# Performance work log

Hardware: AMD Instinct MI355X
Metric: run time of the kernel (lower is better)

The kernel has to match this reference:

```python
import jax, jax.numpy as jnp
import numpy as np

B, L, D = 4, 2048, 512
CHUNK = 64
EPS = 1e-5


def setup_inputs() -> dict:
    key = jax.random.key(0)
    kx, kw = jax.random.split(key)
    x = jax.random.normal(kx, (B, L, D), dtype=jnp.float32)
    W = jax.random.normal(kw, (D, D), dtype=jnp.float32) / np.float32(np.sqrt(D))
    return {
        "x": x,
        "W": W,
        "eta": jnp.asarray(0.01, jnp.float32),
        "lam_logit": jnp.asarray(np.log(0.99 / 0.01), jnp.float32),  # logit(0.99)
        "ln_gamma": jnp.ones((D,), jnp.float32),
        "ln_beta": jnp.zeros((D,), jnp.float32),
    }


def _gated_delta_scan(k, v, q, lam, beta):
    """Gated delta rule: S_t = lam*S_{t-1} + beta * k_t (x) (v_t - lam*S_{t-1}^T k_t);
    o_t = S_t^T q_t (scale=1.0, single head of dim D). k,v,q: [B,L,D] -> o: [B,L,D]."""
    b, l, d = k.shape
    nc = l // CHUNK

    def to_scan(t):  # [B,L,D] -> [nc, CHUNK, B, D]
        return t.transpose(1, 0, 2).reshape(nc, CHUNK, b, d)

    ks, vs, qs = to_scan(k), to_scan(v), to_scan(q)

    def step(S, inp):
        k_t, v_t, q_t = inp                      # each [B,D]
        S = lam * S                              # scalar decay exp(g), g = log(lam)
        v_err = beta * (v_t - jnp.einsum('bk,bkv->bv', k_t, S))
        S = S + k_t[:, :, None] * v_err[:, None, :]
        o_t = jnp.einsum('bk,bkv->bv', q_t, S)
        return S, o_t

    def chunk_body(S, ch):
        return jax.lax.scan(step, S, ch)

    S0 = jnp.zeros((b, d, d), k.dtype)
    _, o = jax.lax.scan(chunk_body, S0, (ks, vs, qs))  # o: [nc, CHUNK, B, D]
    return o.reshape(l, b, d).transpose(1, 0, 2)


def reference(x, W, eta, lam_logit, ln_gamma, ln_beta):
    lam = jax.nn.sigmoid(lam_logit)
    x_act = jnp.tanh(x)
    static_out = jnp.einsum('bld,ed->ble', x_act, W)  # torch Linear (no bias): x @ W.T
    # k = q = tanh(x), v = W @ tanh(x), g = log(lam), beta = eta
    o_dyn = _gated_delta_scan(x_act, static_out, x_act, lam, eta)
    y = static_out + o_dyn
    mu = jnp.mean(y, axis=-1, keepdims=True)
    var = jnp.var(y, axis=-1, keepdims=True)
    return (y - mu) * jax.lax.rsqrt(var + EPS) * ln_gamma + ln_beta
```

## Files before the change

### kernel.cpp

```cpp
#include <hip/hip_runtime.h>
#include <math.h>

#define BB 4
#define LL 2048
#define DD 512
#define CC 64
#define NC 32
#define VB 8
#define EPSF 1e-5f

typedef unsigned int u32;
typedef unsigned short u16;
typedef __attribute__((ext_vector_type(4))) u32 u32x4;
typedef __attribute__((ext_vector_type(4))) float f32x4;
typedef __attribute__((ext_vector_type(8))) __bf16 bf16x8;

__device__ __forceinline__ u16 f2bf(float f) {
  return __builtin_bit_cast(u16, (__bf16)f);
}
__device__ __forceinline__ int sx6(int s) { return (s ^ (s >> 3)) & 7; }
__device__ __forceinline__ bf16x8 ldf(const u16* p) {
  return __builtin_bit_cast(bf16x8, *(const u32x4*)p);
}
__device__ __forceinline__ bf16x8 bcv(u32x4 v) { return __builtin_bit_cast(bf16x8, v); }

__device__ __forceinline__ void gld16(u16* lds, const u16* g) {
  __builtin_amdgcn_global_load_lds(
      (const __attribute__((address_space(1))) u32*)g,
      (__attribute__((address_space(3))) u32*)lds, 16, 0, 0);
}
__device__ __forceinline__ void barrier_lgkm() {
  asm volatile("s_waitcnt lgkmcnt(0)" ::: "memory");
  __builtin_amdgcn_sched_barrier(0);
  __builtin_amdgcn_s_barrier();
  __builtin_amdgcn_sched_barrier(0);
}
__device__ __forceinline__ void barrier_all() {
  asm volatile("s_waitcnt vmcnt(0) lgkmcnt(0)" ::: "memory");
  __builtin_amdgcn_sched_barrier(0);
  __builtin_amdgcn_s_barrier();
  __builtin_amdgcn_sched_barrier(0);
}

__global__ __launch_bounds__(256) void k_tanh(const float* __restrict__ x,
                                              u16* __restrict__ kbs) {
  int row  = blockIdx.x * 4 + (threadIdx.x >> 6);
  int lane = threadIdx.x & 63;
  const float* xr = x + (size_t)row * DD + lane * 8;
  float4 a = *(const float4*)xr;
  float4 b = *(const float4*)(xr + 4);
  float v[8] = {a.x, a.y, a.z, a.w, b.x, b.y, b.z, b.w};
  u32x4 pk;
#pragma unroll
  for (int j = 0; j < 4; ++j) {
    u16 h0 = f2bf(tanhf(v[2 * j]));
    u16 h1 = f2bf(tanhf(v[2 * j + 1]));
    pk[j] = (u32)h0 | ((u32)h1 << 16);
  }
  int s = row & 63;
  int k0 = (lane * 8) ^ (sx6(s) << 3);
  *(u32x4*)(kbs + (size_t)row * DD + k0) = pk;
}

__global__ __launch_bounds__(256) void k_cvtW(const float* __restrict__ W,
                                              u16* __restrict__ wbb) {
  int idx = (blockIdx.x * 256 + threadIdx.x) * 8;
  float4 a = *(const float4*)(W + idx);
  float4 b = *(const float4*)(W + idx + 4);
  float v[8] = {a.x, a.y, a.z, a.w, b.x, b.y, b.z, b.w};
  u32x4 pk;
#pragma unroll
  for (int j = 0; j < 4; ++j)
    pk[j] = (u32)f2bf(v[2 * j]) | ((u32)f2bf(v[2 * j + 1]) << 16);
  *(u32x4*)(wbb + idx) = pk;
}

__global__ __launch_bounds__(256) void k_prep2(const u16* __restrict__ kbs,
                                               const float* __restrict__ eta_p,
                                               const float* __restrict__ ll_p,
                                               u16* __restrict__ tbb,
                                               u16* __restrict__ tcb,
                                               u16* __restrict__ mtb,
                                               u16* __restrict__ kbt) {
  __shared__ __align__(16) u16 Kl[CC * DD];
  __shared__ float Gl[64 * 64];
  __shared__ float Gs[64 * 64];
  __shared__ float Tl[64 * 65];
  __shared__ float pw[72];
  int bc = blockIdx.x;
  int b = bc >> 5, c = bc & 31;
  int tid = threadIdx.x;
  int wid = tid >> 6, lane = tid & 63;
  int lo = lane & 15, hi = lane >> 4;
  float beta = *eta_p;
  float lam = 1.f / (1.f + expf(-*ll_p));
  if (tid <= 64) pw[tid] = powf(lam, (float)tid);
  for (int i = tid; i < 64 * 65; i += 256) Tl[i] = 0.f;
  const u16* Kg = kbs + (size_t)(b * LL + c * CC) * DD;
#pragma unroll
  for (int i = 0; i < 16; ++i)
    gld16(Kl + (size_t)(i * 256 + tid) * 8, Kg + (size_t)(i * 256 + tid) * 8);
  __syncthreads();
  {
    f32x4 acc[4] = {{0.f,0.f,0.f,0.f},{0.f,0.f,0.f,0.f},{0.f,0.f,0.f,0.f},{0.f,0.f,0.f,0.f}};
    int t = 16 * wid + lo;
    int mT = sx6(t) << 3;
#pragma unroll
    for (int kq = 0; kq < 16; ++kq) {
      int col = hi * 8 + kq * 32;
      bf16x8 aF = ldf(Kl + t * DD + (col ^ mT));
#pragma unroll
      for (int sb = 0; sb < 4; ++sb) {
        int s = 16 * sb + lo;
        bf16x8 bF = ldf(Kl + s * DD + (col ^ (sx6(s) << 3)));
        acc[sb] = __builtin_amdgcn_mfma_f32_16x16x32_bf16(aF, bF, acc[sb], 0, 0, 0);
      }
    }
#pragma unroll
    for (int sb = 0; sb < 4; ++sb)
#pragma unroll
      for (int r = 0; r < 4; ++r)
        Gl[(16 * wid + 4 * hi + r) * 64 + 16 * sb + lo] = acc[sb][r];
  }
  __syncthreads();
#pragma unroll
  for (int i = 0; i < 16; ++i) {
    int idx = tid + i * 256;
    int tq = idx >> 6, sq = idx & 63;
    Gs[idx] = (sq < tq) ? beta * pw[tq - sq] * Gl[idx] : 0.f;
  }
  __syncthreads();
  {
    int q = hi;
    int j = 16 * wid + lo;
    for (int t = 0; t < 64; ++t) {
      float ps = 0.f;
#pragma unroll
      for (int i = 0; i < 16; ++i) {
        int s = 16 * q + i;
        ps = fmaf(Gs[t * 64 + s], Tl[s * 65 + j], ps);
      }
      ps += __shfl_xor(ps, 16, 64);
      ps += __shfl_xor(ps, 32, 64);
      if (q == 0) Tl[t * 65 + j] = ((t == j) ? 1.f : 0.f) - ps;
    }
  }
  __syncthreads();
  u16* tb = tbb + (size_t)bc * 64 * 64;
  u16* tc = tcb + (size_t)bc * 64 * 64;
  u16* mt = mtb + (size_t)bc * 64 * 64;
#pragma unroll
  for (int i = 0; i < 16; ++i) {
    int idx = tid + i * 256;
    int s = idx >> 6, r = idx & 63;
    float tv = Tl[s * 65 + r];
    tb[idx] = f2bf(beta * tv);
    tc[idx] = f2bf(-(beta * tv * pw[r + 1]));
    mt[idx] = f2bf((r < s) ? pw[s - r] * Gl[s * 64 + r]
                           : ((r == s) ? Gl[s * 64 + r] : 0.f));
  }
  u16* ktb = kbt + (size_t)bc * CC * DD;
#pragma unroll
  for (int rr = 0; rr < 2; ++rr) {
    int k = rr * 256 + tid;
    int kbase = k & ~7, klo = k & 7;
    int mk = sx6(k) << 3;
#pragma unroll
    for (int g = 0; g < 8; ++g) {
      u32 w4[4];
#pragma unroll
      for (int p = 0; p < 4; ++p) {
        int s0 = g * 8 + 2 * p;
        u16 e0 = Kl[s0 * DD + (kbase ^ (sx6(s0) << 3)) + klo];
        u16 e1 = Kl[(s0 + 1) * DD + (kbase ^ (sx6(s0 + 1) << 3)) + klo];
        w4[p] = (u32)e0 | ((u32)e1 << 16);
      }
      *(u32x4*)(ktb + (size_t)k * 64 + ((8 * g) ^ mk)) = (u32x4){w4[0], w4[1], w4[2], w4[3]};
    }
  }
}

__global__ __launch_bounds__(512, 2) void k_scan6(const u16* __restrict__ kbs,
                                                  const u16* __restrict__ kbt,
                                                  const u16* __restrict__ wbb,
                                                  const u16* __restrict__ tbb,
                                                  const u16* __restrict__ tcb,
                                                  const u16* __restrict__ mtb,
                                                  const float* __restrict__ ll_p,
                                                  float* __restrict__ y) {
  __shared__ __align__(16) u16 Kl[CC * DD];
  __shared__ __align__(16) u16 Sb[16 * DD];
  __shared__ float Vp[2 * 16 * 68];
  __shared__ float Up[2 * 16 * 68];
  __shared__ __align__(16) u16 Vt[16 * 64];
  __shared__ __align__(16) u16 Ut[16 * 64];
  __shared__ __align__(16) u16 Wt[16 * 64];
  __shared__ __align__(16) u16 Ws[16 * 64];

  int b = blockIdx.x >> 6;
  int vb = blockIdx.x & 63;
  int v0 = vb * VB;
  int tid = threadIdx.x;
  int wid = tid >> 6, lane = tid & 63;
  int wq = wid & 3, kh = wid >> 2;
  int lo = lane & 15, hi = lane >> 4;
  int sidx = 16 * wq + lo;
  int mK = sx6(sidx) << 3;
  int mLo = sx6(lo) << 3;
  int kOff = kh * 256;

  float lam = 1.f / (1.f + expf(-*ll_p));
  float lam64 = powf(lam, 64.f);
  float csc = powf(lam, (float)(sidx + 1));
  float dsc = powf(lam, (float)(63 - sidx));

  {
    u32x4 z = {0u, 0u, 0u, 0u};
    *((u32x4*)Sb + tid) = z;
    *((u32x4*)Sb + 512 + tid) = z;
    if (tid < 512) {
      u16* base = (tid >> 7) == 0 ? Vt : (tid >> 7) == 1 ? Ut : (tid >> 7) == 2 ? Wt : Ws;
      *((u32x4*)base + (tid & 127)) = z;
    }
  }
  const u16* kb_b = kbs + (size_t)b * LL * DD;
  float* yb = y + (size_t)b * LL * DD;

  u32x4 wf[8];
#pragma unroll
  for (int kq = 0; kq < 8; ++kq)
    wf[kq] = *(const u32x4*)(wbb + (size_t)((v0 + lo) & 511) * DD + kOff + hi * 8 + kq * 32);

  u32x4 sreg[8];
#pragma unroll
  for (int i = 0; i < 8; ++i)
    sreg[i] = *(const u32x4*)(kb_b + (size_t)(i * 512 + tid) * 8);
  u32x4 kt0[4], kt1[4], tA0, tA1, tB0, tB1;
  {
    const u16* ktc = kbt + (size_t)(b * NC + 0) * CC * DD;
#pragma unroll
    for (int t = 0; t < 4; ++t) {
      int k = 16 * (8 * wq + 4 * kh + t) + lo;
      const u16* rowp = ktc + (size_t)k * 64;
      int m = sx6(k) << 3;
      kt0[t] = *(const u32x4*)(rowp + ((8 * hi) ^ m));
      kt1[t] = *(const u32x4*)(rowp + ((8 * hi + 32) ^ m));
    }
    size_t tbase = ((size_t)(b * NC + 0) * 64 + sidx) * 64 + hi * 8;
    if (kh == 0) {
      tA0 = *(const u32x4*)(tbb + tbase);
      tA1 = *(const u32x4*)(tbb + tbase + 32);
      tB0 = *(const u32x4*)(tcb + tbase);
      tB1 = *(const u32x4*)(tcb + tbase + 32);
    } else {
      tA0 = *(const u32x4*)(mtb + tbase);
      tA1 = *(const u32x4*)(mtb + tbase + 32);
      tB0 = tA0; tB1 = tA1;
    }
  }
#pragma unroll
  for (int i = 0; i < 8; ++i)
    *(u32x4*)(Kl + (size_t)(i * 512 + tid) * 8) = sreg[i];

  f32x4 Sa[4];
#pragma unroll
  for (int t = 0; t < 4; ++t) Sa[t] = (f32x4){0.f, 0.f, 0.f, 0.f};
  barrier_all();

  for (int c = 0; c < NC; ++c) {
    if (c + 1 < NC) {
      const u16* src = kb_b + (size_t)(c + 1) * CC * DD;
#pragma unroll
      for (int i = 0; i < 8; ++i)
        sreg[i] = *(const u32x4*)(src + (size_t)(i * 512 + tid) * 8);
    }
    f32x4 Va0 = {0.f,0.f,0.f,0.f}, Va1 = {0.f,0.f,0.f,0.f};
    f32x4 Ua0 = {0.f,0.f,0.f,0.f}, Ua1 = {0.f,0.f,0.f,0.f};
#pragma unroll
    for (int kq = 0; kq < 8; ++kq) {
      int col = kOff + hi * 8 + kq * 32;
      bf16x8 kB = ldf(Kl + sidx * DD + (col ^ mK));
      bf16x8 sA = ldf(Sb + lo * DD + (col ^ mLo));
      if (kq & 1) {
        Va1 = __builtin_amdgcn_mfma_f32_16x16x32_bf16(bcv(wf[kq]), kB, Va1, 0, 0, 0);
        Ua1 = __builtin_amdgcn_mfma_f32_16x16x32_bf16(sA, kB, Ua1, 0, 0, 0);
      } else {
        Va0 = __builtin_amdgcn_mfma_f32_16x16x32_bf16(bcv(wf[kq]), kB, Va0, 0, 0, 0);
        Ua0 = __builtin_amdgcn_mfma_f32_16x16x32_bf16(sA, kB, Ua0, 0, 0, 0);
      }
    }
#pragma unroll
    for (int r = 0; r < 4; ++r) {
      int v = 4 * hi + r;
      Vp[(kh * 16 + v) * 68 + sidx] = Va0[r] + Va1[r];
      Up[(kh * 16 + v) * 68 + sidx] = Ua0[r] + Ua1[r];
    }
    barrier_lgkm();
    if (c + 1 < NC) {
#pragma unroll
      for (int i = 0; i < 8; ++i)
        *(u32x4*)(Kl + (size_t)(i * 512 + tid) * 8) = sreg[i];
    }
    float VaF[4], UaF[4];
#pragma unroll
    for (int r = 0; r < 4; ++r) {
      int v = 4 * hi + r;
      VaF[r] = Vp[v * 68 + sidx] + Vp[(16 + v) * 68 + sidx];
      UaF[r] = Up[v * 68 + sidx] + Up[(16 + v) * 68 + sidx];
    }
    if (kh == 0 && hi < 2) {
#pragma unroll
      for (int r = 0; r < 4; ++r) {
        int v = 4 * hi + r;
        int idx = v * 64 + (sidx ^ (sx6(v) << 3));
        Vt[idx] = f2bf(VaF[r]);
        Ut[idx] = f2bf(UaF[r]);
      }
    }
    barrier_lgkm();
    if (kh == 0) {
      bf16x8 vf0 = ldf(Vt + lo * 64 + ((hi * 8) ^ mLo));
      bf16x8 vf1 = ldf(Vt + lo * 64 + ((hi * 8 + 32) ^ mLo));
      bf16x8 uf0 = ldf(Ut + lo * 64 + ((hi * 8) ^ mLo));
      bf16x8 uf1 = ldf(Ut + lo * 64 + ((hi * 8 + 32) ^ mLo));
      f32x4 Wa0 = {0.f,0.f,0.f,0.f}, Wa1 = {0.f,0.f,0.f,0.f};
      Wa0 = __builtin_amdgcn_mfma_f32_16x16x32_bf16(vf0, bcv(tA0), Wa0, 0, 0, 0);
      Wa1 = __builtin_amdgcn_mfma_f32_16x16x32_bf16(vf1, bcv(tA1), Wa1, 0, 0, 0);
      Wa0 = __builtin_amdgcn_mfma_f32_16x16x32_bf16(uf0, bcv(tB0), Wa0, 0, 0, 0);
      Wa1 = __builtin_amdgcn_mfma_f32_16x16x32_bf16(uf1, bcv(tB1), Wa1, 0, 0, 0);
      f32x4 Wa = Wa0 + Wa1;
      if (hi < 2) {
#pragma unroll
        for (int r = 0; r < 4; ++r) {
          int v = 4 * hi + r;
          int idx = v * 64 + (sidx ^ (sx6(v) << 3));
          Wt[idx] = f2bf(Wa[r]);
          Ws[idx] = f2bf(Wa[r] * dsc);
        }
      }
    }
    barrier_lgkm();
    if (kh == 1) {
      f32x4 Oa;
#pragma unroll
      for (int r = 0; r < 4; ++r) Oa[r] = csc * UaF[r];
      bf16x8 wff0 = ldf(Wt + lo * 64 + ((hi * 8) ^ mLo));
      bf16x8 wff1 = ldf(Wt + lo * 64 + ((hi * 8 + 32) ^ mLo));
      Oa = __builtin_amdgcn_mfma_f32_16x16x32_bf16(wff0, bcv(tA0), Oa, 0, 0, 0);
      Oa = __builtin_amdgcn_mfma_f32_16x16x32_bf16(wff1, bcv(tA1), Oa, 0, 0, 0);
      if (hi < 2) {
        float4 yo = make_float4(VaF[0] + Oa[0], VaF[1] + Oa[1],
                                VaF[2] + Oa[2], VaF[3] + Oa[3]);
        *(float4*)(yb + (size_t)(c * CC + sidx) * DD + v0 + 4 * hi) = yo;
      }
    }
    {
      bf16x8 ws0 = ldf(Ws + lo * 64 + ((hi * 8) ^ mLo));
      bf16x8 ws1 = ldf(Ws + lo * 64 + ((hi * 8 + 32) ^ mLo));
#pragma unroll
      for (int t = 0; t < 4; ++t) {
        f32x4 acc = Sa[t] * lam64;
        acc = __builtin_amdgcn_mfma_f32_16x16x32_bf16(ws0, bcv(kt0[t]), acc, 0, 0, 0);
        acc = __builtin_amdgcn_mfma_f32_16x16x32_bf16(ws1, bcv(kt1[t]), acc, 0, 0, 0);
        Sa[t] = acc;
      }
      if (hi < 2) {
#pragma unroll
        for (int t = 0; t < 4; ++t) {
          int kc = 16 * (8 * wq + 4 * kh + t) + lo;
#pragma unroll
          for (int r = 0; r < 4; ++r) {
            int v = 4 * hi + r;
            Sb[v * DD + (kc ^ (sx6(v) << 3))] = f2bf(Sa[t][r]);
          }
        }
      }
    }
    if (c + 1 < NC) {
      const u16* ktc = kbt + (size_t)(b * NC + c + 1) * CC * DD;
#pragma unroll
      for (int t = 0; t < 4; ++t) {
        int k = 16 * (8 * wq + 4 * kh + t) + lo;
        const u16* rowp = ktc + (size_t)k * 64;
        int m = sx6(k) << 3;
        kt0[t] = *(const u32x4*)(rowp + ((8 * hi) ^ m));
        kt1[t] = *(const u32x4*)(rowp + ((8 * hi + 32) ^ m));
      }
      size_t tbase = ((size_t)(b * NC + c + 1) * 64 + sidx) * 64 + hi * 8;
      if (kh == 0) {
        tA0 = *(const u32x4*)(tbb + tbase);
        tA1 = *(const u32x4*)(tbb + tbase + 32);
        tB0 = *(const u32x4*)(tcb + tbase);
        tB1 = *(const u32x4*)(tcb + tbase + 32);
      } else {
        tA0 = *(const u32x4*)(mtb + tbase);
        tA1 = *(const u32x4*)(mtb + tbase + 32);
      }
    }
    barrier_lgkm();
  }
}

__global__ __launch_bounds__(256) void k_ln(float* __restrict__ y,
                                            const float* __restrict__ gamma,
                                            const float* __restrict__ lbeta) {
  int row = blockIdx.x * 4 + (threadIdx.x >> 6);
  int lane = threadIdx.x & 63;
  float* yr = y + (size_t)row * DD + lane * 8;
  float4 a = *(const float4*)yr;
  float4 b = *(const float4*)(yr + 4);
  float v[8] = {a.x, a.y, a.z, a.w, b.x, b.y, b.z, b.w};
  float s = 0.f, ss = 0.f;
#pragma unroll
  for (int j = 0; j < 8; ++j) {
    s += v[j];
    ss = fmaf(v[j], v[j], ss);
  }
#pragma unroll
  for (int m = 1; m < 64; m <<= 1) {
    s += __shfl_xor(s, m, 64);
    ss += __shfl_xor(ss, m, 64);
  }
  float mu = s * (1.f / DD);
  float var = ss * (1.f / DD) - mu * mu;
  float inv = rsqrtf(var + EPSF);
  const float* gp = gamma + lane * 8;
  const float* bp = lbeta + lane * 8;
  float4 g0 = *(const float4*)gp;
  float4 g1 = *(const float4*)(gp + 4);
  float4 b0 = *(const float4*)bp;
  float4 b1 = *(const float4*)(bp + 4);
  float g[8] = {g0.x, g0.y, g0.z, g0.w, g1.x, g1.y, g1.z, g1.w};
  float bb[8] = {b0.x, b0.y, b0.z, b0.w, b1.x, b1.y, b1.z, b1.w};
#pragma unroll
  for (int j = 0; j < 8; ++j) v[j] = (v[j] - mu) * inv * g[j] + bb[j];
  *(float4*)yr = make_float4(v[0], v[1], v[2], v[3]);
  *(float4*)(yr + 4) = make_float4(v[4], v[5], v[6], v[7]);
}

extern "C" void kernel_launch(void* const* d_in, const int* in_sizes, int n_in,
                              void* d_out, int out_size, void* d_ws, size_t ws_size,
                              hipStream_t stream) {
  const float* x     = (const float*)d_in[0];
  const float* W     = (const float*)d_in[1];
  const float* eta   = (const float*)d_in[2];
  const float* ll    = (const float*)d_in[3];
  const float* gamma = (const float*)d_in[4];
  const float* lbeta = (const float*)d_in[5];
  float* out = (float*)d_out;

  u16* kbs = (u16*)d_ws;
  u16* kbt = kbs + (size_t)BB * LL * DD;
  u16* wbb = kbt + (size_t)BB * LL * DD;
  u16* tbb = wbb + (size_t)DD * DD;
  u16* tcb = tbb + (size_t)BB * NC * 64 * 64;
  u16* mtb = tcb + (size_t)BB * NC * 64 * 64;

  k_tanh<<<2048, 256, 0, stream>>>(x, kbs);
  k_cvtW<<<128, 256, 0, stream>>>(W, wbb);
  k_prep2<<<BB * NC, 256, 0, stream>>>(kbs, eta, ll, tbb, tcb, mtb, kbt);
  k_scan6<<<256, 512, 0, stream>>>(kbs, kbt, wbb, tbb, tcb, mtb, ll, out);
  k_ln<<<2048, 256, 0, stream>>>(out, gamma, lbeta);
}
```

Measured before the change: 148.9 us.

## Double scan block to 1024 threads and hoist next-chunk V projection off critical path

The scan kernel now runs 16 waves per block instead of 8, splitting the K dimension four ways (128 columns each) and reducing partial sums across four slices in shared memory. The projection V = W·k for the next chunk is computed early, after the current chunk's U/V reduction, so only the S·k product stays on the serial per-chunk path. This roughly halves per-wave MFMA and register work per chunk. In exchange it adds a wider cross-wave reduction, a larger shared buffer, and more threads at each barrier.

```diff
diff --git a/kernel.cpp b/kernel.cpp
--- a/kernel.cpp
+++ b/kernel.cpp
@@ -180,18 +180,18 @@
   }
 }
 
-__global__ __launch_bounds__(512, 2) void k_scan6(const u16* __restrict__ kbs,
-                                                  const u16* __restrict__ kbt,
-                                                  const u16* __restrict__ wbb,
-                                                  const u16* __restrict__ tbb,
-                                                  const u16* __restrict__ tcb,
-                                                  const u16* __restrict__ mtb,
-                                                  const float* __restrict__ ll_p,
-                                                  float* __restrict__ y) {
+__global__ __launch_bounds__(1024, 4) void k_scan7(const u16* __restrict__ kbs,
+                                                   const u16* __restrict__ kbt,
+                                                   const u16* __restrict__ wbb,
+                                                   const u16* __restrict__ tbb,
+                                                   const u16* __restrict__ tcb,
+                                                   const u16* __restrict__ mtb,
+                                                   const float* __restrict__ ll_p,
+                                                   float* __restrict__ y) {
   __shared__ __align__(16) u16 Kl[CC * DD];
   __shared__ __align__(16) u16 Sb[16 * DD];
-  __shared__ float Vp[2 * 16 * 68];
-  __shared__ float Up[2 * 16 * 68];
+  __shared__ float Vp[4 * 16 * 68];
+  __shared__ float Up[4 * 16 * 68];
   __shared__ __align__(16) u16 Vt[16 * 64];
   __shared__ __align__(16) u16 Ut[16 * 64];
   __shared__ __align__(16) u16 Wt[16 * 64];
@@ -207,7 +207,7 @@
   int sidx = 16 * wq + lo;
   int mK = sx6(sidx) << 3;
   int mLo = sx6(lo) << 3;
-  int kOff = kh * 256;
+  int kOff = kh * 128;
 
   float lam = 1.f / (1.f + expf(-*ll_p));
   float lam64 = powf(lam, 64.f);
@@ -217,30 +217,30 @@
   {
     u32x4 z = {0u, 0u, 0u, 0u};
     *((u32x4*)Sb + tid) = z;
-    *((u32x4*)Sb + 512 + tid) = z;
     if (tid < 512) {
-      u16* base = (tid >> 7) == 0 ? Vt : (tid >> 7) == 1 ? Ut : (tid >> 7) == 2 ? Wt : Ws;
+      u16* base = (tid >> 7) == 0 ? Vt : (tid >> 7) == 1 ? Ut
+                : (tid >> 7) == 2 ? Wt : Ws;
       *((u32x4*)base + (tid & 127)) = z;
     }
   }
   const u16* kb_b = kbs + (size_t)b * LL * DD;
   float* yb = y + (size_t)b * LL * DD;
 
-  u32x4 wf[8];
-#pragma unroll
-  for (int kq = 0; kq < 8; ++kq)
+  u32x4 wf[4];
+#pragma unroll
+  for (int kq = 0; kq < 4; ++kq)
     wf[kq] = *(const u32x4*)(wbb + (size_t)((v0 + lo) & 511) * DD + kOff + hi * 8 + kq * 32);
 
-  u32x4 sreg[8];
-#pragma unroll
-  for (int i = 0; i < 8; ++i)
-    sreg[i] = *(const u32x4*)(kb_b + (size_t)(i * 512 + tid) * 8);
-  u32x4 kt0[4], kt1[4], tA0, tA1, tB0, tB1;
+  u32x4 sreg[4];
+#pragma unroll
+  for (int i = 0; i < 4; ++i)
+    sreg[i] = *(const u32x4*)(kb_b + (size_t)(i * 1024 + tid) * 8);
+  u32x4 kt0[2], kt1[2], tA0, tA1, tB0, tB1;
   {
     const u16* ktc = kbt + (size_t)(b * NC + 0) * CC * DD;
 #pragma unroll
-    for (int t = 0; t < 4; ++t) {
-      int k = 16 * (8 * wq + 4 * kh + t) + lo;
+    for (int t = 0; t < 2; ++t) {
+      int k = 16 * (2 * wid + t) + lo;
       const u16* rowp = ktc + (size_t)k * 64;
       int m = sx6(k) << 3;
       kt0[t] = *(const u32x4*)(rowp + ((8 * hi) ^ m));
@@ -259,62 +259,75 @@
     }
   }
 #pragma unroll
-  for (int i = 0; i < 8; ++i)
-    *(u32x4*)(Kl + (size_t)(i * 512 + tid) * 8) = sreg[i];
-
-  f32x4 Sa[4];
-#pragma unroll
-  for (int t = 0; t < 4; ++t) Sa[t] = (f32x4){0.f, 0.f, 0.f, 0.f};
+  for (int i = 0; i < 4; ++i)
+    *(u32x4*)(Kl + (size_t)(i * 1024 + tid) * 8) = sreg[i];
+
+  f32x4 Sa[2];
+  Sa[0] = (f32x4){0.f, 0.f, 0.f, 0.f};
+  Sa[1] = (f32x4){0.f, 0.f, 0.f, 0.f};
   barrier_all();
+
+  {
+    f32x4 Va0 = {0.f,0.f,0.f,0.f}, Va1 = {0.f,0.f,0.f,0.f};
+#pragma unroll
+    for (int kq = 0; kq < 4; ++kq) {
+      int col = kOff + hi * 8 + kq * 32;
+      bf16x8 kB = ldf(Kl + sidx * DD + (col ^ mK));
+      if (kq & 1) Va1 = __builtin_amdgcn_mfma_f32_16x16x32_bf16(bcv(wf[kq]), kB, Va1, 0, 0, 0);
+      else        Va0 = __builtin_amdgcn_mfma_f32_16x16x32_bf16(bcv(wf[kq]), kB, Va0, 0, 0, 0);
+    }
+    f32x4 Va = Va0 + Va1;
+#pragma unroll
+    for (int r = 0; r < 4; ++r)
+      Vp[(kh * 16 + 4 * hi + r) * 68 + sidx] = Va[r];
+  }
 
   for (int c = 0; c < NC; ++c) {
     if (c + 1 < NC) {
       const u16* src = kb_b + (size_t)(c + 1) * CC * DD;
 #pragma unroll
-      for (int i = 0; i < 8; ++i)
-        sreg[i] = *(const u32x4*)(src + (size_t)(i * 512 + tid) * 8);
-    }
-    f32x4 Va0 = {0.f,0.f,0.f,0.f}, Va1 = {0.f,0.f,0.f,0.f};
-    f32x4 Ua0 = {0.f,0.f,0.f,0.f}, Ua1 = {0.f,0.f,0.f,0.f};
-#pragma unroll
-    for (int kq = 0; kq < 8; ++kq) {
-      int col = kOff + hi * 8 + kq * 32;
-      bf16x8 kB = ldf(Kl + sidx * DD + (col ^ mK));
-      bf16x8 sA = ldf(Sb + lo * DD + (col ^ mLo));
-      if (kq & 1) {
-        Va1 = __builtin_amdgcn_mfma_f32_16x16x32_bf16(bcv(wf[kq]), kB, Va1, 0, 0, 0);
-        Ua1 = __builtin_amdgcn_mfma_f32_16x16x32_bf16(sA, kB, Ua1, 0, 0, 0);
-      } else {
-        Va0 = __builtin_amdgcn_mfma_f32_16x16x32_bf16(bcv(wf[kq]), kB, Va0, 0, 0, 0);
-        Ua0 = __builtin_amdgcn_mfma_f32_16x16x32_bf16(sA, kB, Ua0, 0, 0, 0);
-      }
-    }
-#pragma unroll
-    for (int r = 0; r < 4; ++r) {
-      int v = 4 * hi + r;
-      Vp[(kh * 16 + v) * 68 + sidx] = Va0[r] + Va1[r];
-      Up[(kh * 16 + v) * 68 + sidx] = Ua0[r] + Ua1[r];
+      for (int i = 0; i < 4; ++i)
+        sreg[i] = *(const u32x4*)(src + (size_t)(i * 1024 + tid) * 8);
+    }
+    {
+      f32x4 Ua0 = {0.f,0.f,0.f,0.f}, Ua1 = {0.f,0.f,0.f,0.f};
+#pragma unroll
+      for (int kq = 0; kq < 4; ++kq) {
+        int col = kOff + hi * 8 + kq * 32;
+        bf16x8 kB = ldf(Kl + sidx * DD + (col ^ mK));
+        bf16x8 sA = ldf(Sb + lo * DD + (col ^ mLo));
+        if (kq & 1) Ua1 = __builtin_amdgcn_mfma_f32_16x16x32_bf16(sA, kB, Ua1, 0, 0, 0);
+        else        Ua0 = __builtin_amdgcn_mfma_f32_16x16x32_bf16(sA, kB, Ua0, 0, 0, 0);
+      }
+      f32x4 Ua = Ua0 + Ua1;
+#pragma unroll
+      for (int r = 0; r < 4; ++r)
+        Up[(kh * 16 + 4 * hi + r) * 68 + sidx] = Ua[r];
     }
     barrier_lgkm();
     if (c + 1 < NC) {
 #pragma unroll
-      for (int i = 0; i < 8; ++i)
-        *(u32x4*)(Kl + (size_t)(i * 512 + tid) * 8) = sreg[i];
-    }
-    float VaF[4], UaF[4];
-#pragma unroll
-    for (int r = 0; r < 4; ++r) {
-      int v = 4 * hi + r;
-      VaF[r] = Vp[v * 68 + sidx] + Vp[(16 + v) * 68 + sidx];
-      UaF[r] = Up[v * 68 + sidx] + Up[(16 + v) * 68 + sidx];
-    }
-    if (kh == 0 && hi < 2) {
+      for (int i = 0; i < 4; ++i)
+        *(u32x4*)(Kl + (size_t)(i * 1024 + tid) * 8) = sreg[i];
+    }
+    float UaF[4], VaF[4];
+    if (kh < 2) {
 #pragma unroll
       for (int r = 0; r < 4; ++r) {
         int v = 4 * hi + r;
-        int idx = v * 64 + (sidx ^ (sx6(v) << 3));
-        Vt[idx] = f2bf(VaF[r]);
-        Ut[idx] = f2bf(UaF[r]);
+        UaF[r] = (Up[v * 68 + sidx] + Up[(16 + v) * 68 + sidx]) +
+                 (Up[(32 + v) * 68 + sidx] + Up[(48 + v) * 68 + sidx]);
+        VaF[r] = (Vp[v * 68 + sidx] + Vp[(16 + v) * 68 + sidx]) +
+                 (Vp[(32 + v) * 68 + sidx] + Vp[(48 + v) * 68 + sidx]);
+      }
+      if (kh == 0 && hi < 2) {
+#pragma unroll
+        for (int r = 0; r < 4; ++r) {
+          int v = 4 * hi + r;
+          int idx = v * 64 + (sidx ^ (sx6(v) << 3));
+          Ut[idx] = f2bf(UaF[r]);
+          Vt[idx] = f2bf(VaF[r]);
+        }
       }
     }
     barrier_lgkm();
@@ -339,6 +352,20 @@
         }
       }
     }
+    if (c + 1 < NC) {
+      f32x4 Va0 = {0.f,0.f,0.f,0.f}, Va1 = {0.f,0.f,0.f,0.f};
+#pragma unroll
+      for (int kq = 0; kq < 4; ++kq) {
+        int col = kOff + hi * 8 + kq * 32;
+        bf16x8 kB = ldf(Kl + sidx * DD + (col ^ mK));
+        if (kq & 1) Va1 = __builtin_amdgcn_mfma_f32_16x16x32_bf16(bcv(wf[kq]), kB, Va1, 0, 0, 0);
+        else        Va0 = __builtin_amdgcn_mfma_f32_16x16x32_bf16(bcv(wf[kq]), kB, Va0, 0, 0, 0);
+      }
+      f32x4 Va = Va0 + Va1;
+#pragma unroll
+      for (int r = 0; r < 4; ++r)
+        Vp[(kh * 16 + 4 * hi + r) * 68 + sidx] = Va[r];
+    }
     barrier_lgkm();
     if (kh == 1) {
       f32x4 Oa;
@@ -358,7 +385,7 @@
       bf16x8 ws0 = ldf(Ws + lo * 64 + ((hi * 8) ^ mLo));
       bf16x8 ws1 = ldf(Ws + lo * 64 + ((hi * 8 + 32) ^ mLo));
 #pragma unroll
-      for (int t = 0; t < 4; ++t) {
+      for (int t = 0; t < 2; ++t) {
         f32x4 acc = Sa[t] * lam64;
         acc = __builtin_amdgcn_mfma_f32_16x16x32_bf16(ws0, bcv(kt0[t]), acc, 0, 0, 0);
         acc = __builtin_amdgcn_mfma_f32_16x16x32_bf16(ws1, bcv(kt1[t]), acc, 0, 0, 0);
@@ -366,8 +393,8 @@
       }
       if (hi < 2) {
 #pragma unroll
-        for (int t = 0; t < 4; ++t) {
-          int kc = 16 * (8 * wq + 4 * kh + t) + lo;
+        for (int t = 0; t < 2; ++t) {
+          int kc = 16 * (2 * wid + t) + lo;
 #pragma unroll
           for (int r = 0; r < 4; ++r) {
             int v = 4 * hi + r;
@@ -379,8 +406,8 @@
     if (c + 1 < NC) {
       const u16* ktc = kbt + (size_t)(b * NC + c + 1) * CC * DD;
 #pragma unroll
-      for (int t = 0; t < 4; ++t) {
-        int k = 16 * (8 * wq + 4 * kh + t) + lo;
+      for (int t = 0; t < 2; ++t) {
+        int k = 16 * (2 * wid + t) + lo;
         const u16* rowp = ktc + (size_t)k * 64;
         int m = sx6(k) << 3;
         kt0[t] = *(const u32x4*)(rowp + ((8 * hi) ^ m));
@@ -392,7 +419,7 @@
         tA1 = *(const u32x4*)(tbb + tbase + 32);
         tB0 = *(const u32x4*)(tcb + tbase);
         tB1 = *(const u32x4*)(tcb + tbase + 32);
-      } else {
+      } else if (kh == 1) {
         tA0 = *(const u32x4*)(mtb + tbase);
         tA1 = *(const u32x4*)(mtb + tbase + 32);
       }
@@ -459,6 +486,6 @@
   k_tanh<<<2048, 256, 0, stream>>>(x, kbs);
   k_cvtW<<<128, 256, 0, stream>>>(W, wbb);
   k_prep2<<<BB * NC, 256, 0, stream>>>(kbs, eta, ll, tbb, tcb, mtb, kbt);
-  k_scan6<<<256, 512, 0, stream>>>(kbs, kbt, wbb, tbb, tcb, mtb, ll, out);
+  k_scan7<<<256, 1024, 0, stream>>>(kbs, kbt, wbb, tbb, tcb, mtb, ll, out);
   k_ln<<<2048, 256, 0, stream>>>(out, gamma, lbeta);
 }
```

After: 409.5 us. +175.1%, slower.

## Fuse tanh into prep, precompute chunk output matrices, shorten scan critical path

Applied to the files above, without the earlier changes.

The tanh/bf16 conversion kernel is folded into the per-chunk prep kernel, which now writes the K buffer and keeps it in LDS, removing one launch and a global round trip. The prep kernel also precomputes the products of the masked Gram matrix with the T matrices (P1, P2) and folds the decay scale into T. This lets the scan kernel compute the chunk output directly from V and U in parallel with the state update weights, removing one barrier-separated serial stage and the Wt buffer. The V projection for the next chunk is moved into the current iteration so it overlaps other work. The cost is more precompute and extra bf16 rounding of the precomputed products.

```diff
diff --git a/kernel.cpp b/kernel.cpp
--- a/kernel.cpp
+++ b/kernel.cpp
@@ -24,11 +24,6 @@
 }
 __device__ __forceinline__ bf16x8 bcv(u32x4 v) { return __builtin_bit_cast(bf16x8, v); }
 
-__device__ __forceinline__ void gld16(u16* lds, const u16* g) {
-  __builtin_amdgcn_global_load_lds(
-      (const __attribute__((address_space(1))) u32*)g,
-      (__attribute__((address_space(3))) u32*)lds, 16, 0, 0);
-}
 __device__ __forceinline__ void barrier_lgkm() {
   asm volatile("s_waitcnt lgkmcnt(0)" ::: "memory");
   __builtin_amdgcn_sched_barrier(0);
@@ -40,26 +35,6 @@
   __builtin_amdgcn_sched_barrier(0);
   __builtin_amdgcn_s_barrier();
   __builtin_amdgcn_sched_barrier(0);
-}
-
-__global__ __launch_bounds__(256) void k_tanh(const float* __restrict__ x,
-                                              u16* __restrict__ kbs) {
-  int row  = blockIdx.x * 4 + (threadIdx.x >> 6);
-  int lane = threadIdx.x & 63;
-  const float* xr = x + (size_t)row * DD + lane * 8;
-  float4 a = *(const float4*)xr;
-  float4 b = *(const float4*)(xr + 4);
-  float v[8] = {a.x, a.y, a.z, a.w, b.x, b.y, b.z, b.w};
-  u32x4 pk;
-#pragma unroll
-  for (int j = 0; j < 4; ++j) {
-    u16 h0 = f2bf(tanhf(v[2 * j]));
-    u16 h1 = f2bf(tanhf(v[2 * j + 1]));
-    pk[j] = (u32)h0 | ((u32)h1 << 16);
-  }
-  int s = row & 63;
-  int k0 = (lane * 8) ^ (sx6(s) << 3);
-  *(u32x4*)(kbs + (size_t)row * DD + k0) = pk;
 }
 
 __global__ __launch_bounds__(256) void k_cvtW(const float* __restrict__ W,
@@ -75,17 +50,22 @@
   *(u32x4*)(wbb + idx) = pk;
 }
 
-__global__ __launch_bounds__(256) void k_prep2(const u16* __restrict__ kbs,
+__global__ __launch_bounds__(256) void k_prep3(const float* __restrict__ x,
                                                const float* __restrict__ eta_p,
                                                const float* __restrict__ ll_p,
-                                               u16* __restrict__ tbb,
-                                               u16* __restrict__ tcb,
-                                               u16* __restrict__ mtb,
+                                               u16* __restrict__ kbs,
+                                               u16* __restrict__ tbs,
+                                               u16* __restrict__ tcs,
+                                               u16* __restrict__ p1g,
+                                               u16* __restrict__ p2g,
                                                u16* __restrict__ kbt) {
   __shared__ __align__(16) u16 Kl[CC * DD];
   __shared__ float Gl[64 * 64];
   __shared__ float Gs[64 * 64];
   __shared__ float Tl[64 * 65];
+  __shared__ __align__(16) u16 MtL[64 * 64];
+  __shared__ __align__(16) u16 TbT[64 * 64];
+  __shared__ __align__(16) u16 TcT[64 * 64];
   __shared__ float pw[72];
   int bc = blockIdx.x;
   int b = bc >> 5, c = bc & 31;
@@ -96,10 +76,24 @@
   float lam = 1.f / (1.f + expf(-*ll_p));
   if (tid <= 64) pw[tid] = powf(lam, (float)tid);
   for (int i = tid; i < 64 * 65; i += 256) Tl[i] = 0.f;
-  const u16* Kg = kbs + (size_t)(b * LL + c * CC) * DD;
-#pragma unroll
-  for (int i = 0; i < 16; ++i)
-    gld16(Kl + (size_t)(i * 256 + tid) * 8, Kg + (size_t)(i * 256 + tid) * 8);
+  const float* xg = x + (size_t)(b * LL + c * CC) * DD;
+  u16* kbs_c = kbs + (size_t)(b * LL + c * CC) * DD;
+#pragma unroll
+  for (int i = 0; i < 16; ++i) {
+    int idx = tid + i * 256;
+    int r = idx >> 6, k8 = (idx & 63) * 8;
+    const float* xp = xg + (size_t)r * DD + k8;
+    float4 a = *(const float4*)xp;
+    float4 b4 = *(const float4*)(xp + 4);
+    float v[8] = {a.x, a.y, a.z, a.w, b4.x, b4.y, b4.z, b4.w};
+    u32x4 pk;
+#pragma unroll
+    for (int j = 0; j < 4; ++j)
+      pk[j] = (u32)f2bf(tanhf(v[2 * j])) | ((u32)f2bf(tanhf(v[2 * j + 1])) << 16);
+    int off = r * DD + (k8 ^ (sx6(r) << 3));
+    *(u32x4*)(Kl + off) = pk;
+    *(u32x4*)(kbs_c + off) = pk;
+  }
   __syncthreads();
   {
     f32x4 acc[4] = {{0.f,0.f,0.f,0.f},{0.f,0.f,0.f,0.f},{0.f,0.f,0.f,0.f},{0.f,0.f,0.f,0.f}};
@@ -146,18 +140,59 @@
     }
   }
   __syncthreads();
-  u16* tb = tbb + (size_t)bc * 64 * 64;
-  u16* tc = tcb + (size_t)bc * 64 * 64;
-  u16* mt = mtb + (size_t)bc * 64 * 64;
+  u16* tbso = tbs + (size_t)bc * 4096;
+  u16* tcso = tcs + (size_t)bc * 4096;
 #pragma unroll
   for (int i = 0; i < 16; ++i) {
     int idx = tid + i * 256;
     int s = idx >> 6, r = idx & 63;
     float tv = Tl[s * 65 + r];
-    tb[idx] = f2bf(beta * tv);
-    tc[idx] = f2bf(-(beta * tv * pw[r + 1]));
-    mt[idx] = f2bf((r < s) ? pw[s - r] * Gl[s * 64 + r]
-                           : ((r == s) ? Gl[s * 64 + r] : 0.f));
+    float sc = pw[63 - s] * beta;
+    tbso[idx] = f2bf(sc * tv);
+    tcso[idx] = f2bf(-sc * pw[r + 1] * tv);
+    int swz = r ^ (sx6(s) << 3);
+    float mtv = (r < s) ? pw[s - r] * Gl[s * 64 + r]
+                        : ((r == s) ? Gl[s * 64 + r] : 0.f);
+    MtL[s * 64 + swz] = f2bf(mtv);
+    float tvT = Tl[r * 65 + s];
+    TbT[s * 64 + swz] = f2bf(beta * tvT);
+    TcT[s * 64 + swz] = f2bf(-beta * pw[s + 1] * tvT);
+  }
+  __syncthreads();
+  {
+    f32x4 p1a[4], p2a[4];
+#pragma unroll
+    for (int rt = 0; rt < 4; ++rt) {
+      p1a[rt] = (f32x4){0.f, 0.f, 0.f, 0.f};
+      p2a[rt] = (f32x4){0.f, 0.f, 0.f, 0.f};
+    }
+    int srow = 16 * wid + lo;
+    int aswz = sx6(srow) << 3;
+#pragma unroll
+    for (int km = 0; km < 2; ++km) {
+      int mo = hi * 8 + km * 32;
+      bf16x8 aF = ldf(MtL + srow * 64 + (mo ^ aswz));
+#pragma unroll
+      for (int rt = 0; rt < 4; ++rt) {
+        int rrow = 16 * rt + lo;
+        int bswz = sx6(rrow) << 3;
+        p1a[rt] = __builtin_amdgcn_mfma_f32_16x16x32_bf16(
+            aF, ldf(TbT + rrow * 64 + (mo ^ bswz)), p1a[rt], 0, 0, 0);
+        p2a[rt] = __builtin_amdgcn_mfma_f32_16x16x32_bf16(
+            aF, ldf(TcT + rrow * 64 + (mo ^ bswz)), p2a[rt], 0, 0, 0);
+      }
+    }
+    u16* p1o = p1g + (size_t)bc * 4096;
+    u16* p2o = p2g + (size_t)bc * 4096;
+#pragma unroll
+    for (int rt = 0; rt < 4; ++rt)
+#pragma unroll
+      for (int rg = 0; rg < 4; ++rg) {
+        int s = 16 * wid + 4 * hi + rg;
+        int r = 16 * rt + lo;
+        p1o[s * 64 + r] = f2bf(p1a[rt][rg]);
+        p2o[s * 64 + r] = f2bf(p2a[rt][rg]);
+      }
   }
   u16* ktb = kbt + (size_t)bc * CC * DD;
 #pragma unroll
@@ -180,12 +215,13 @@
   }
 }
 
-__global__ __launch_bounds__(512, 2) void k_scan6(const u16* __restrict__ kbs,
+__global__ __launch_bounds__(512, 2) void k_scan8(const u16* __restrict__ kbs,
                                                   const u16* __restrict__ kbt,
                                                   const u16* __restrict__ wbb,
-                                                  const u16* __restrict__ tbb,
-                                                  const u16* __restrict__ tcb,
-                                                  const u16* __restrict__ mtb,
+                                                  const u16* __restrict__ tbs,
+                                                  const u16* __restrict__ tcs,
+                                                  const u16* __restrict__ p1g,
+                                                  const u16* __restrict__ p2g,
                                                   const float* __restrict__ ll_p,
                                                   float* __restrict__ y) {
   __shared__ __align__(16) u16 Kl[CC * DD];
@@ -194,7 +230,6 @@
   __shared__ float Up[2 * 16 * 68];
   __shared__ __align__(16) u16 Vt[16 * 64];
   __shared__ __align__(16) u16 Ut[16 * 64];
-  __shared__ __align__(16) u16 Wt[16 * 64];
   __shared__ __align__(16) u16 Ws[16 * 64];
 
   int b = blockIdx.x >> 6;
@@ -212,14 +247,13 @@
   float lam = 1.f / (1.f + expf(-*ll_p));
   float lam64 = powf(lam, 64.f);
   float csc = powf(lam, (float)(sidx + 1));
-  float dsc = powf(lam, (float)(63 - sidx));
 
   {
     u32x4 z = {0u, 0u, 0u, 0u};
     *((u32x4*)Sb + tid) = z;
     *((u32x4*)Sb + 512 + tid) = z;
-    if (tid < 512) {
-      u16* base = (tid >> 7) == 0 ? Vt : (tid >> 7) == 1 ? Ut : (tid >> 7) == 2 ? Wt : Ws;
+    if (tid < 384) {
+      u16* base = (tid >> 7) == 0 ? Vt : (tid >> 7) == 1 ? Ut : Ws;
       *((u32x4*)base + (tid & 127)) = z;
     }
   }
@@ -235,28 +269,24 @@
 #pragma unroll
   for (int i = 0; i < 8; ++i)
     sreg[i] = *(const u32x4*)(kb_b + (size_t)(i * 512 + tid) * 8);
-  u32x4 kt0[4], kt1[4], tA0, tA1, tB0, tB1;
+  u32x4 kt0[4], kt1[4], fA0, fA1, fB0, fB1;
   {
     const u16* ktc = kbt + (size_t)(b * NC + 0) * CC * DD;
 #pragma unroll
     for (int t = 0; t < 4; ++t) {
-      int k = 16 * (8 * wq + 4 * kh + t) + lo;
+      int k = 16 * (4 * wid + t) + lo;
       const u16* rowp = ktc + (size_t)k * 64;
       int m = sx6(k) << 3;
       kt0[t] = *(const u32x4*)(rowp + ((8 * hi) ^ m));
       kt1[t] = *(const u32x4*)(rowp + ((8 * hi + 32) ^ m));
     }
     size_t tbase = ((size_t)(b * NC + 0) * 64 + sidx) * 64 + hi * 8;
-    if (kh == 0) {
-      tA0 = *(const u32x4*)(tbb + tbase);
-      tA1 = *(const u32x4*)(tbb + tbase + 32);
-      tB0 = *(const u32x4*)(tcb + tbase);
-      tB1 = *(const u32x4*)(tcb + tbase + 32);
-    } else {
-      tA0 = *(const u32x4*)(mtb + tbase);
-      tA1 = *(const u32x4*)(mtb + tbase + 32);
-      tB0 = tA0; tB1 = tA1;
-    }
+    const u16* mA = (kh == 0) ? tbs : p1g;
+    const u16* mB = (kh == 0) ? tcs : p2g;
+    fA0 = *(const u32x4*)(mA + tbase);
+    fA1 = *(const u32x4*)(mA + tbase + 32);
+    fB0 = *(const u32x4*)(mB + tbase);
+    fB1 = *(const u32x4*)(mB + tbase + 32);
   }
 #pragma unroll
   for (int i = 0; i < 8; ++i)
@@ -266,6 +296,21 @@
 #pragma unroll
   for (int t = 0; t < 4; ++t) Sa[t] = (f32x4){0.f, 0.f, 0.f, 0.f};
   barrier_all();
+
+  {
+    f32x4 Va0 = {0.f,0.f,0.f,0.f}, Va1 = {0.f,0.f,0.f,0.f};
+#pragma unroll
+    for (int kq = 0; kq < 8; ++kq) {
+      int col = kOff + hi * 8 + kq * 32;
+      bf16x8 kB = ldf(Kl + sidx * DD + (col ^ mK));
+      if (kq & 1) Va1 = __builtin_amdgcn_mfma_f32_16x16x32_bf16(bcv(wf[kq]), kB, Va1, 0, 0, 0);
+      else        Va0 = __builtin_amdgcn_mfma_f32_16x16x32_bf16(bcv(wf[kq]), kB, Va0, 0, 0, 0);
+    }
+    f32x4 Va = Va0 + Va1;
+#pragma unroll
+    for (int r = 0; r < 4; ++r)
+      Vp[(kh * 16 + 4 * hi + r) * 68 + sidx] = Va[r];
+  }
 
   for (int c = 0; c < NC; ++c) {
     if (c + 1 < NC) {
@@ -274,86 +319,93 @@
       for (int i = 0; i < 8; ++i)
         sreg[i] = *(const u32x4*)(src + (size_t)(i * 512 + tid) * 8);
     }
-    f32x4 Va0 = {0.f,0.f,0.f,0.f}, Va1 = {0.f,0.f,0.f,0.f};
-    f32x4 Ua0 = {0.f,0.f,0.f,0.f}, Ua1 = {0.f,0.f,0.f,0.f};
-#pragma unroll
-    for (int kq = 0; kq < 8; ++kq) {
-      int col = kOff + hi * 8 + kq * 32;
-      bf16x8 kB = ldf(Kl + sidx * DD + (col ^ mK));
-      bf16x8 sA = ldf(Sb + lo * DD + (col ^ mLo));
-      if (kq & 1) {
-        Va1 = __builtin_amdgcn_mfma_f32_16x16x32_bf16(bcv(wf[kq]), kB, Va1, 0, 0, 0);
-        Ua1 = __builtin_amdgcn_mfma_f32_16x16x32_bf16(sA, kB, Ua1, 0, 0, 0);
-      } else {
-        Va0 = __builtin_amdgcn_mfma_f32_16x16x32_bf16(bcv(wf[kq]), kB, Va0, 0, 0, 0);
-        Ua0 = __builtin_amdgcn_mfma_f32_16x16x32_bf16(sA, kB, Ua0, 0, 0, 0);
-      }
-    }
+    {
+      f32x4 Ua0 = {0.f,0.f,0.f,0.f}, Ua1 = {0.f,0.f,0.f,0.f};
+#pragma unroll
+      for (int kq = 0; kq < 8; ++kq) {
+        int col = kOff + hi * 8 + kq * 32;
+        bf16x8 kB = ldf(Kl + sidx * DD + (col ^ mK));
+        bf16x8 sA = ldf(Sb + lo * DD + (col ^ mLo));
+        if (kq & 1) Ua1 = __builtin_amdgcn_mfma_f32_16x16x32_bf16(sA, kB, Ua1, 0, 0, 0);
+        else        Ua0 = __builtin_amdgcn_mfma_f32_16x16x32_bf16(sA, kB, Ua0, 0, 0, 0);
+      }
+      f32x4 Ua = Ua0 + Ua1;
+#pragma unroll
+      for (int r = 0; r < 4; ++r)
+        Up[(kh * 16 + 4 * hi + r) * 68 + sidx] = Ua[r];
+    }
+    barrier_lgkm();
+    if (c + 1 < NC) {
+#pragma unroll
+      for (int i = 0; i < 8; ++i)
+        *(u32x4*)(Kl + (size_t)(i * 512 + tid) * 8) = sreg[i];
+    }
+    float UaF[4], VaF[4];
 #pragma unroll
     for (int r = 0; r < 4; ++r) {
       int v = 4 * hi + r;
-      Vp[(kh * 16 + v) * 68 + sidx] = Va0[r] + Va1[r];
-      Up[(kh * 16 + v) * 68 + sidx] = Ua0[r] + Ua1[r];
-    }
-    barrier_lgkm();
-    if (c + 1 < NC) {
-#pragma unroll
-      for (int i = 0; i < 8; ++i)
-        *(u32x4*)(Kl + (size_t)(i * 512 + tid) * 8) = sreg[i];
-    }
-    float VaF[4], UaF[4];
-#pragma unroll
-    for (int r = 0; r < 4; ++r) {
-      int v = 4 * hi + r;
+      UaF[r] = Up[v * 68 + sidx] + Up[(16 + v) * 68 + sidx];
       VaF[r] = Vp[v * 68 + sidx] + Vp[(16 + v) * 68 + sidx];
-      UaF[r] = Up[v * 68 + sidx] + Up[(16 + v) * 68 + sidx];
     }
     if (kh == 0 && hi < 2) {
 #pragma unroll
       for (int r = 0; r < 4; ++r) {
         int v = 4 * hi + r;
         int idx = v * 64 + (sidx ^ (sx6(v) << 3));
+        Ut[idx] = f2bf(UaF[r]);
         Vt[idx] = f2bf(VaF[r]);
-        Ut[idx] = f2bf(UaF[r]);
       }
     }
     barrier_lgkm();
-    if (kh == 0) {
+    {
       bf16x8 vf0 = ldf(Vt + lo * 64 + ((hi * 8) ^ mLo));
       bf16x8 vf1 = ldf(Vt + lo * 64 + ((hi * 8 + 32) ^ mLo));
       bf16x8 uf0 = ldf(Ut + lo * 64 + ((hi * 8) ^ mLo));
       bf16x8 uf1 = ldf(Ut + lo * 64 + ((hi * 8 + 32) ^ mLo));
-      f32x4 Wa0 = {0.f,0.f,0.f,0.f}, Wa1 = {0.f,0.f,0.f,0.f};
-      Wa0 = __builtin_amdgcn_mfma_f32_16x16x32_bf16(vf0, bcv(tA0), Wa0, 0, 0, 0);
-      Wa1 = __builtin_amdgcn_mfma_f32_16x16x32_bf16(vf1, bcv(tA1), Wa1, 0, 0, 0);
-      Wa0 = __builtin_amdgcn_mfma_f32_16x16x32_bf16(uf0, bcv(tB0), Wa0, 0, 0, 0);
-      Wa1 = __builtin_amdgcn_mfma_f32_16x16x32_bf16(uf1, bcv(tB1), Wa1, 0, 0, 0);
-      f32x4 Wa = Wa0 + Wa1;
-      if (hi < 2) {
-#pragma unroll
-        for (int r = 0; r < 4; ++r) {
-          int v = 4 * hi + r;
-          int idx = v * 64 + (sidx ^ (sx6(v) << 3));
-          Wt[idx] = f2bf(Wa[r]);
-          Ws[idx] = f2bf(Wa[r] * dsc);
+      if (kh == 0) {
+        f32x4 Wa0 = {0.f,0.f,0.f,0.f}, Wa1 = {0.f,0.f,0.f,0.f};
+        Wa0 = __builtin_amdgcn_mfma_f32_16x16x32_bf16(vf0, bcv(fA0), Wa0, 0, 0, 0);
+        Wa1 = __builtin_amdgcn_mfma_f32_16x16x32_bf16(vf1, bcv(fA1), Wa1, 0, 0, 0);
+        Wa0 = __builtin_amdgcn_mfma_f32_16x16x32_bf16(uf0, bcv(fB0), Wa0, 0, 0, 0);
+        Wa1 = __builtin_amdgcn_mfma_f32_16x16x32_bf16(uf1, bcv(fB1), Wa1, 0, 0, 0);
+        f32x4 Wa = Wa0 + Wa1;
+        if (hi < 2) {
+#pragma unroll
+          for (int r = 0; r < 4; ++r) {
+            int v = 4 * hi + r;
+            Ws[v * 64 + (sidx ^ (sx6(v) << 3))] = f2bf(Wa[r]);
+          }
         }
-      }
+      } else {
+        f32x4 Oa, Ob = {0.f,0.f,0.f,0.f};
+#pragma unroll
+        for (int r = 0; r < 4; ++r) Oa[r] = csc * UaF[r];
+        Oa = __builtin_amdgcn_mfma_f32_16x16x32_bf16(vf0, bcv(fA0), Oa, 0, 0, 0);
+        Ob = __builtin_amdgcn_mfma_f32_16x16x32_bf16(vf1, bcv(fA1), Ob, 0, 0, 0);
+        Oa = __builtin_amdgcn_mfma_f32_16x16x32_bf16(uf0, bcv(fB0), Oa, 0, 0, 0);
+        Ob = __builtin_amdgcn_mfma_f32_16x16x32_bf16(uf1, bcv(fB1), Ob, 0, 0, 0);
+        if (hi < 2) {
+          float4 yo = make_float4(VaF[0] + Oa[0] + Ob[0], VaF[1] + Oa[1] + Ob[1],
+                                  VaF[2] + Oa[2] + Ob[2], VaF[3] + Oa[3] + Ob[3]);
+          *(float4*)(yb + (size_t)(c * CC + sidx) * DD + v0 + 4 * hi) = yo;
+        }
+      }
+    }
+    if (c + 1 < NC) {
+      f32x4 Va0 = {0.f,0.f,0.f,0.f}, Va1 = {0.f,0.f,0.f,0.f};
+#pragma unroll
+      for (int kq = 0; kq < 8; ++kq) {
+        int col = kOff + hi * 8 + kq * 32;
+        bf16x8 kB = ldf(Kl + sidx * DD + (col ^ mK));
+        if (kq & 1) Va1 = __builtin_amdgcn_mfma_f32_16x16x32_bf16(bcv(wf[kq]), kB, Va1, 0, 0, 0);
+        else        Va0 = __builtin_amdgcn_mfma_f32_16x16x32_bf16(bcv(wf[kq]), kB, Va0, 0, 0, 0);
+      }
+      f32x4 Va = Va0 + Va1;
+#pragma unroll
+      for (int r = 0; r < 4; ++r)
+        Vp[(kh * 16 + 4 * hi + r) * 68 + sidx] = Va[r];
     }
     barrier_lgkm();
-    if (kh == 1) {
-      f32x4 Oa;
-#pragma unroll
-      for (int r = 0; r < 4; ++r) Oa[r] = csc * UaF[r];
-      bf16x8 wff0 = ldf(Wt + lo * 64 + ((hi * 8) ^ mLo));
-      bf16x8 wff1 = ldf(Wt + lo * 64 + ((hi * 8 + 32) ^ mLo));
-      Oa = __builtin_amdgcn_mfma_f32_16x16x32_bf16(wff0, bcv(tA0), Oa, 0, 0, 0);
-      Oa = __builtin_amdgcn_mfma_f32_16x16x32_bf16(wff1, bcv(tA1), Oa, 0, 0, 0);
-      if (hi < 2) {
-        float4 yo = make_float4(VaF[0] + Oa[0], VaF[1] + Oa[1],
-                                VaF[2] + Oa[2], VaF[3] + Oa[3]);
-        *(float4*)(yb + (size_t)(c * CC + sidx) * DD + v0 + 4 * hi) = yo;
-      }
-    }
     {
       bf16x8 ws0 = ldf(Ws + lo * 64 + ((hi * 8) ^ mLo));
       bf16x8 ws1 = ldf(Ws + lo * 64 + ((hi * 8 + 32) ^ mLo));
@@ -367,7 +419,7 @@
       if (hi < 2) {
 #pragma unroll
         for (int t = 0; t < 4; ++t) {
-          int kc = 16 * (8 * wq + 4 * kh + t) + lo;
+          int kc = 16 * (4 * wid + t) + lo;
 #pragma unroll
           for (int r = 0; r < 4; ++r) {
             int v = 4 * hi + r;
@@ -380,22 +432,19 @@
       const u16* ktc = kbt + (size_t)(b * NC + c + 1) * CC * DD;
 #pragma unroll
       for (int t = 0; t < 4; ++t) {
-        int k = 16 * (8 * wq + 4 * kh + t) + lo;
+        int k = 16 * (4 * wid + t) + lo;
         const u16* rowp = ktc + (size_t)k * 64;
         int m = sx6(k) << 3;
         kt0[t] = *(const u32x4*)(rowp + ((8 * hi) ^ m));
         kt1[t] = *(const u32x4*)(rowp + ((8 * hi + 32) ^ m));
       }
       size_t tbase = ((size_t)(b * NC + c + 1) * 64 + sidx) * 64 + hi * 8;
-      if (kh == 0) {
-        tA0 = *(const u32x4*)(tbb + tbase);
-        tA1 = *(const u32x4*)(tbb + tbase + 32);
-        tB0 = *(const u32x4*)(tcb + tbase);
-        tB1 = *(const u32x4*)(tcb + tbase + 32);
-      } else {
-        tA0 = *(const u32x4*)(mtb + tbase);
-        tA1 = *(const u32x4*)(mtb + tbase + 32);
-      }
+      const u16* mA = (kh == 0) ? tbs : p1g;
+      const u16* mB = (kh == 0) ? tcs : p2g;
+      fA0 = *(const u32x4*)(mA + tbase);
+      fA1 = *(const u32x4*)(mA + tbase + 32);
+      fB0 = *(const u32x4*)(mB + tbase);
+      fB1 = *(const u32x4*)(mB + tbase + 32);
     }
     barrier_lgkm();
   }
@@ -452,13 +501,13 @@
   u16* kbs = (u16*)d_ws;
   u16* kbt = kbs + (size_t)BB * LL * DD;
   u16* wbb = kbt + (size_t)BB * LL * DD;
-  u16* tbb = wbb + (size_t)DD * DD;
-  u16* tcb = tbb + (size_t)BB * NC * 64 * 64;
-  u16* mtb = tcb + (size_t)BB * NC * 64 * 64;
-
-  k_tanh<<<2048, 256, 0, stream>>>(x, kbs);
+  u16* tbs = wbb + (size_t)DD * DD;
+  u16* tcs = tbs + (size_t)BB * NC * 64 * 64;
+  u16* p1g = tcs + (size_t)BB * NC * 64 * 64;
+  u16* p2g = p1g + (size_t)BB * NC * 64 * 64;
+
   k_cvtW<<<128, 256, 0, stream>>>(W, wbb);
-  k_prep2<<<BB * NC, 256, 0, stream>>>(kbs, eta, ll, tbb, tcb, mtb, kbt);
-  k_scan6<<<256, 512, 0, stream>>>(kbs, kbt, wbb, tbb, tcb, mtb, ll, out);
+  k_prep3<<<BB * NC, 256, 0, stream>>>(x, eta, ll, kbs, tbs, tcs, p1g, p2g, kbt);
+  k_scan8<<<256, 512, 0, stream>>>(kbs, kbt, wbb, tbs, tcs, p1g, p2g, ll, out);
   k_ln<<<2048, 256, 0, stream>>>(out, gamma, lbeta);
 }
```

Result: slower. 173.3 us (+16.4%).
